# Kernel optimization log

Measured on AMD Instinct MI355X. Metric: run time of the kernel, lower is better.

## Reference

```python
import jax, jax.numpy as jnp
import numpy as np

B, T, N, U = 16, 512, 2048, 64  # batch_size, dim1, dim2 (=nodes), units


def setup_inputs() -> dict:
    key = jax.random.key(0)
    k1, k2, k3, k4 = jax.random.split(key, 4)
    x = jax.random.normal(k1, (B, T, N), dtype=jnp.float32)
    Adj = jax.random.uniform(k2, (N, N), dtype=jnp.float32)
    W = jax.random.normal(k3, (U, N), dtype=jnp.float32) * 0.05  # 'uniform' init stand-in
    b = jax.random.normal(k4, (U,), dtype=jnp.float32) * 0.05
    return {"x": x, "Adj": Adj, "W": W, "b": b}


def reference(x, Adj, W, b):
    # Original loop: out_i[b,t,j] = sum_k x[b,t,k] * Adj[j,k] * W[i,k] + b[i],
    # then mean over i. By linearity this equals a single matmul with the
    # unit-averaged weight vector and the averaged bias.
    w_bar = jnp.mean(W, axis=0)              # [N]
    w_eff = Adj * w_bar                       # [N(j), N(k)] : Adj[j,k] * w_bar[k]
    out = jnp.einsum('btk,jk->btj', x, w_eff) + jnp.mean(b)
    return out  # [B, T, N]
```

## Files before the change

### kernel.cpp

```cpp
#include <hip/hip_runtime.h>

#define N_DIM 2048
#define U_DIM 64
#define M_DIM 8192
#define K_DIM 2048

typedef __bf16 bf16x8 __attribute__((ext_vector_type(8)));
typedef float  floatx4 __attribute__((ext_vector_type(4)));
typedef unsigned short ushort8 __attribute__((ext_vector_type(8)));

#define AS1 __attribute__((address_space(1)))
#define AS3 __attribute__((address_space(3)))

__device__ __forceinline__ unsigned short f_to_bf16_rne(float f) {
    unsigned int x;
    __builtin_memcpy(&x, &f, 4);
    x += 0x7fffu + ((x >> 16) & 1u);
    return (unsigned short)(x >> 16);
}

__global__ __launch_bounds__(256) void prep_kernel(
    const float* __restrict__ W, const float* __restrict__ b,
    float* __restrict__ wbar, float* __restrict__ bmean) {
    int k = blockIdx.x * 256 + threadIdx.x;
    float s = 0.f;
#pragma unroll
    for (int i = 0; i < U_DIM; ++i) s += W[i * N_DIM + k];
    wbar[k] = s * (1.f / U_DIM);

    if (blockIdx.x == 0 && threadIdx.x < 64) {
        float v = b[threadIdx.x];
#pragma unroll
        for (int off = 32; off > 0; off >>= 1) v += __shfl_down(v, off);
        if (threadIdx.x == 0) bmean[0] = v * (1.f / U_DIM);
    }
}

__global__ __launch_bounds__(256) void weff_convx_kernel(
    const float* __restrict__ Adj, const float* __restrict__ wbar,
    unsigned short* __restrict__ weff,
    const float* __restrict__ x, unsigned short* __restrict__ xbf) {
    if (blockIdx.x < 2048) {
        long long idx = ((long long)blockIdx.x * 256 + threadIdx.x) * 8;
        int k = (int)(idx & (N_DIM - 1));
        floatx4 a0 = *(const floatx4*)(Adj + idx);
        floatx4 a1 = *(const floatx4*)(Adj + idx + 4);
        floatx4 w0 = *(const floatx4*)(wbar + k);
        floatx4 w1 = *(const floatx4*)(wbar + k + 4);
        ushort8 ov;
#pragma unroll
        for (int j = 0; j < 4; ++j) {
            ov[j]     = f_to_bf16_rne(a0[j] * w0[j]);
            ov[j + 4] = f_to_bf16_rne(a1[j] * w1[j]);
        }
        *(ushort8*)(weff + idx) = ov;
    } else {
        long long idx = ((long long)(blockIdx.x - 2048) * 256 + threadIdx.x) * 8;
        floatx4 a0 = *(const floatx4*)(x + idx);
        floatx4 a1 = *(const floatx4*)(x + idx + 4);
        ushort8 ov;
#pragma unroll
        for (int j = 0; j < 4; ++j) {
            ov[j]     = f_to_bf16_rne(a0[j]);
            ov[j + 4] = f_to_bf16_rne(a1[j]);
        }
        *(ushort8*)(xbf + idx) = ov;
    }
}

__global__ __launch_bounds__(256) void convx_kernel(
    const float* __restrict__ x, unsigned short* __restrict__ xbf) {
    long long idx = ((long long)blockIdx.x * 256 + threadIdx.x) * 8;
    floatx4 a0 = *(const floatx4*)(x + idx);
    floatx4 a1 = *(const floatx4*)(x + idx + 4);
    ushort8 ov;
#pragma unroll
    for (int j = 0; j < 4; ++j) {
        ov[j]     = f_to_bf16_rne(a0[j]);
        ov[j + 4] = f_to_bf16_rne(a1[j]);
    }
    *(ushort8*)(xbf + idx) = ov;
}

#define BM 256
#define BN 256
#define BK 64
#define NT (K_DIM / BK)

__global__ __launch_bounds__(512, 2) void gemm_bt_kernel(
    const unsigned short* __restrict__ A,
    const unsigned short* __restrict__ Bt,
    const float* __restrict__ bmeanp,
    float* __restrict__ C,
    int mtiles) {
    __shared__ __align__(16) unsigned short sA[2][BM * BK];
    __shared__ __align__(16) unsigned short sB[2][BN * BK];

    const int id   = blockIdx.x;
    const int nt   = id & 7;
    const int mt   = id >> 3;
    const int tile_m = mt * BM;
    const int tile_n = nt * BN;

    const int tid  = threadIdx.x;
    const int w    = tid >> 6;
    const int lane = tid & 63;
    const int wm   = w >> 2;
    const int wn   = w & 3;

    const float bmean = bmeanp[0];

    const int srow = lane >> 3;
    const int skc  = (lane & 7) ^ srow;
    const unsigned short* gA0 = A  + (size_t)(tile_m + w * 32 + srow) * K_DIM + skc * 8;
    const unsigned short* gB0 = Bt + (size_t)(tile_n + w * 32 + srow) * K_DIM + skc * 8;

    const int fr = lane & 15;
    const int fq = lane >> 4;
    int aoff[2], boff[2];
#pragma unroll
    for (int s = 0; s < 2; ++s) {
        int slot = ((s * 4 + fq) ^ (fr & 7)) * 8;
        aoff[s] = (wm * 128 + fr) * BK + slot;
        boff[s] = (wn * 64 + fr) * BK + slot;
    }

    floatx4 acc[8][4];
#pragma unroll
    for (int mi = 0; mi < 8; ++mi)
#pragma unroll
        for (int ni = 0; ni < 4; ++ni) acc[mi][ni] = (floatx4){0.f, 0.f, 0.f, 0.f};

    #define STAGE(p, kt)                                                          \
        do {                                                                      \
            const int koff_ = (kt) * BK;                                          \
            _Pragma("unroll")                                                     \
            for (int i_ = 0; i_ < 4; ++i_) {                                      \
                __builtin_amdgcn_global_load_lds(                                 \
                    (const AS1 void*)(gA0 + koff_ + (size_t)i_ * 8 * K_DIM),      \
                    (AS3 void*)(&sA[(p)][(w * 4 + i_) * 8 * BK]), 16, 0, 0);      \
                __builtin_amdgcn_global_load_lds(                                 \
                    (const AS1 void*)(gB0 + koff_ + (size_t)i_ * 8 * K_DIM),      \
                    (AS3 void*)(&sB[(p)][(w * 4 + i_) * 8 * BK]), 16, 0, 0);      \
            }                                                                     \
        } while (0)

    STAGE(0, 0);
    STAGE(1, 1);

    for (int t = 0; t < NT; ++t) {
        const int p = t & 1;

        if (t == NT - 1) asm volatile("s_waitcnt vmcnt(0)" ::: "memory");
        else             asm volatile("s_waitcnt vmcnt(8)" ::: "memory");
        __builtin_amdgcn_s_barrier();

#pragma unroll
        for (int s = 0; s < 2; ++s) {
            bf16x8 af[8], bfr[4];
#pragma unroll
            for (int mi = 0; mi < 8; ++mi)
                af[mi] = *(const bf16x8*)&sA[p][aoff[s] + mi * 16 * BK];
#pragma unroll
            for (int ni = 0; ni < 4; ++ni)
                bfr[ni] = *(const bf16x8*)&sB[p][boff[s] + ni * 16 * BK];
            asm volatile("s_waitcnt lgkmcnt(0)" ::: "memory");
            __builtin_amdgcn_sched_barrier(0);
            __builtin_amdgcn_s_setprio(1);
#pragma unroll
            for (int mi = 0; mi < 8; ++mi)
#pragma unroll
                for (int ni = 0; ni < 4; ++ni)
                    acc[mi][ni] = __builtin_amdgcn_mfma_f32_16x16x32_bf16(
                        af[mi], bfr[ni], acc[mi][ni], 0, 0, 0);
            __builtin_amdgcn_s_setprio(0);
        }

        __builtin_amdgcn_s_barrier();

        if (t + 2 < NT) STAGE(p, t + 2);
    }
    #undef STAGE

    const int crow = tile_m + wm * 128 + fq * 4;
    const int ccol = tile_n + wn * 64 + fr;
#pragma unroll
    for (int mi = 0; mi < 8; ++mi)
#pragma unroll
        for (int ni = 0; ni < 4; ++ni)
#pragma unroll
            for (int r = 0; r < 4; ++r) {
                int gm = crow + mi * 16 + r;
                int gn = ccol + ni * 16;
                C[(size_t)gm * N_DIM + gn] = acc[mi][ni][r] + bmean;
            }
    (void)mtiles;
}

extern "C" void kernel_launch(void* const* d_in, const int* in_sizes, int n_in,
                              void* d_out, int out_size, void* d_ws, size_t ws_size,
                              hipStream_t stream) {
    (void)in_sizes; (void)n_in; (void)out_size;
    const float* x   = (const float*)d_in[0];
    const float* Adj = (const float*)d_in[1];
    const float* W   = (const float*)d_in[2];
    const float* b   = (const float*)d_in[3];
    float* out = (float*)d_out;

    char* ws = (char*)d_ws;
    float* wbar  = (float*)ws;
    float* bmean = (float*)(ws + 8192);
    unsigned short* weff = (unsigned short*)(ws + 16384);
    const size_t weff_bytes = (size_t)N_DIM * N_DIM * 2;
    const size_t xbf_off = 16384 + weff_bytes;
    unsigned short* xbf = (unsigned short*)(ws + xbf_off);

    size_t avail = (ws_size > xbf_off) ? (ws_size - xbf_off) : 0;
    long long max_rows = (long long)(avail / ((size_t)K_DIM * 2)) / BM * BM;
    if (max_rows < BM) max_rows = BM;
    if (max_rows > M_DIM) max_rows = M_DIM;

    prep_kernel<<<N_DIM / 256, 256, 0, stream>>>(W, b, wbar, bmean);

    if (max_rows == M_DIM) {
        weff_convx_kernel<<<2048 + M_DIM, 256, 0, stream>>>(Adj, wbar, weff, x, xbf);
        gemm_bt_kernel<<<(M_DIM / BM) * (N_DIM / BN), 512, 0, stream>>>(
            xbf, weff, bmean, out, M_DIM / BM);
    } else {
        weff_convx_kernel<<<2048, 256, 0, stream>>>(Adj, wbar, weff, x, xbf);
        for (long long m0 = 0; m0 < M_DIM; m0 += max_rows) {
            long long rows = (M_DIM - m0 < max_rows) ? (M_DIM - m0) : max_rows;
            convx_kernel<<<(int)rows, 256, 0, stream>>>(x + m0 * K_DIM, xbf);
            gemm_bt_kernel<<<(int)(rows / BM) * (N_DIM / BN), 512, 0, stream>>>(
                xbf, weff, bmean, out + m0 * (size_t)N_DIM, (int)(rows / BM));
        }
    }
}
```

Baseline: 224.5 us.

## Interleave LDS fragment reads with MFMA groups and issue next stage early

Splits each K-tile's work into four MFMA groups and interleaves the LDS fragment loads for the next group with the current group's MFMAs, so LDS latency overlaps with matrix math. The last MFMA group runs after the barrier and after the global-to-LDS prefetch is issued, so the next stage's loads start earlier. This raises register pressure (more fragments live at once) and relies on sched_barrier placement, which may cause spills or lower occupancy at 2 blocks per CU.

```diff
diff --git a/kernel.cpp b/kernel.cpp
--- a/kernel.cpp
+++ b/kernel.cpp
@@ -155,30 +155,71 @@
         else             asm volatile("s_waitcnt vmcnt(8)" ::: "memory");
         __builtin_amdgcn_s_barrier();
 
-#pragma unroll
-        for (int s = 0; s < 2; ++s) {
-            bf16x8 af[8], bfr[4];
-#pragma unroll
-            for (int mi = 0; mi < 8; ++mi)
-                af[mi] = *(const bf16x8*)&sA[p][aoff[s] + mi * 16 * BK];
-#pragma unroll
-            for (int ni = 0; ni < 4; ++ni)
-                bfr[ni] = *(const bf16x8*)&sB[p][boff[s] + ni * 16 * BK];
-            asm volatile("s_waitcnt lgkmcnt(0)" ::: "memory");
-            __builtin_amdgcn_sched_barrier(0);
-            __builtin_amdgcn_s_setprio(1);
-#pragma unroll
-            for (int mi = 0; mi < 8; ++mi)
-#pragma unroll
-                for (int ni = 0; ni < 4; ++ni)
-                    acc[mi][ni] = __builtin_amdgcn_mfma_f32_16x16x32_bf16(
-                        af[mi], bfr[ni], acc[mi][ni], 0, 0, 0);
-            __builtin_amdgcn_s_setprio(0);
-        }
-
+        bf16x8 bf0[4], bf1[4], afa[4], afb[4], afc[4], afd[4];
+
+#pragma unroll
+        for (int ni = 0; ni < 4; ++ni)
+            bf0[ni] = *(const bf16x8*)&sB[p][boff[0] + ni * 16 * BK];
+#pragma unroll
+        for (int i = 0; i < 4; ++i)
+            afa[i] = *(const bf16x8*)&sA[p][aoff[0] + i * 16 * BK];
+        __builtin_amdgcn_sched_barrier(0);
+
+#pragma unroll
+        for (int i = 0; i < 4; ++i)
+            afb[i] = *(const bf16x8*)&sA[p][aoff[0] + (4 + i) * 16 * BK];
+#pragma unroll
+        for (int ni = 0; ni < 4; ++ni)
+            bf1[ni] = *(const bf16x8*)&sB[p][boff[1] + ni * 16 * BK];
+        __builtin_amdgcn_sched_barrier(0);
+        __builtin_amdgcn_s_setprio(1);
+#pragma unroll
+        for (int mi = 0; mi < 4; ++mi)
+#pragma unroll
+            for (int ni = 0; ni < 4; ++ni)
+                acc[mi][ni] = __builtin_amdgcn_mfma_f32_16x16x32_bf16(
+                    afa[mi], bf0[ni], acc[mi][ni], 0, 0, 0);
+        __builtin_amdgcn_s_setprio(0);
+
+#pragma unroll
+        for (int i = 0; i < 4; ++i)
+            afc[i] = *(const bf16x8*)&sA[p][aoff[1] + i * 16 * BK];
+        __builtin_amdgcn_sched_barrier(0);
+        __builtin_amdgcn_s_setprio(1);
+#pragma unroll
+        for (int mi = 4; mi < 8; ++mi)
+#pragma unroll
+            for (int ni = 0; ni < 4; ++ni)
+                acc[mi][ni] = __builtin_amdgcn_mfma_f32_16x16x32_bf16(
+                    afb[mi - 4], bf0[ni], acc[mi][ni], 0, 0, 0);
+        __builtin_amdgcn_s_setprio(0);
+
+#pragma unroll
+        for (int i = 0; i < 4; ++i)
+            afd[i] = *(const bf16x8*)&sA[p][aoff[1] + (4 + i) * 16 * BK];
+        __builtin_amdgcn_sched_barrier(0);
+        __builtin_amdgcn_s_setprio(1);
+#pragma unroll
+        for (int mi = 0; mi < 4; ++mi)
+#pragma unroll
+            for (int ni = 0; ni < 4; ++ni)
+                acc[mi][ni] = __builtin_amdgcn_mfma_f32_16x16x32_bf16(
+                    afc[mi], bf1[ni], acc[mi][ni], 0, 0, 0);
+        __builtin_amdgcn_s_setprio(0);
+
+        asm volatile("s_waitcnt lgkmcnt(0)" ::: "memory");
+        __builtin_amdgcn_sched_barrier(0);
         __builtin_amdgcn_s_barrier();
-
         if (t + 2 < NT) STAGE(p, t + 2);
+        __builtin_amdgcn_sched_barrier(0);
+        __builtin_amdgcn_s_setprio(1);
+#pragma unroll
+        for (int mi = 4; mi < 8; ++mi)
+#pragma unroll
+            for (int ni = 0; ni < 4; ++ni)
+                acc[mi][ni] = __builtin_amdgcn_mfma_f32_16x16x32_bf16(
+                    afd[mi - 4], bf1[ni], acc[mi][ni], 0, 0, 0);
+        __builtin_amdgcn_s_setprio(0);
     }
     #undef STAGE
 
```

Result: faster. 217.4 us (-3.2%).

## Split GEMM main loop into four quadrant phases with interleaved half-tile prefetch

Applied to the files above, without the earlier changes.

Restructures the bf16 GEMM inner loop into four MFMA phases over 4x2 sub-quadrants of each warp's accumulator tile. Global-to-LDS loads for the next k-tile are issued in half-tile chunks spread across the phases, and LDS fragment reads are interleaved between them, in the style of ping-pong scheduling. The goal is to hide load latency and smooth out memory traffic against MFMA execution. In exchange it adds many more barriers per iteration and more complex vmcnt/lgkmcnt accounting, which carries a correctness risk.

```diff
diff --git a/kernel.cpp b/kernel.cpp
--- a/kernel.cpp
+++ b/kernel.cpp
@@ -112,8 +112,8 @@
 
     const int srow = lane >> 3;
     const int skc  = (lane & 7) ^ srow;
-    const unsigned short* gA0 = A  + (size_t)(tile_m + w * 32 + srow) * K_DIM + skc * 8;
-    const unsigned short* gB0 = Bt + (size_t)(tile_n + w * 32 + srow) * K_DIM + skc * 8;
+    const unsigned short* gA = A  + (size_t)(tile_m + w * 16 + srow) * K_DIM + skc * 8;
+    const unsigned short* gB = Bt + (size_t)(tile_n + w * 16 + srow) * K_DIM + skc * 8;
 
     const int fr = lane & 15;
     const int fq = lane >> 4;
@@ -131,56 +131,134 @@
 #pragma unroll
         for (int ni = 0; ni < 4; ++ni) acc[mi][ni] = (floatx4){0.f, 0.f, 0.f, 0.f};
 
-    #define STAGE(p, kt)                                                          \
-        do {                                                                      \
-            const int koff_ = (kt) * BK;                                          \
-            _Pragma("unroll")                                                     \
-            for (int i_ = 0; i_ < 4; ++i_) {                                      \
-                __builtin_amdgcn_global_load_lds(                                 \
-                    (const AS1 void*)(gA0 + koff_ + (size_t)i_ * 8 * K_DIM),      \
-                    (AS3 void*)(&sA[(p)][(w * 4 + i_) * 8 * BK]), 16, 0, 0);      \
-                __builtin_amdgcn_global_load_lds(                                 \
-                    (const AS1 void*)(gB0 + koff_ + (size_t)i_ * 8 * K_DIM),      \
-                    (AS3 void*)(&sB[(p)][(w * 4 + i_) * 8 * BK]), 16, 0, 0);      \
-            }                                                                     \
+    #define STAGE_A_HALF(p, kt, h)                                                 \
+        do {                                                                       \
+            const int ko_ = (kt) * BK;                                             \
+            _Pragma("unroll")                                                      \
+            for (int u_ = 0; u_ < 2; ++u_) {                                       \
+                __builtin_amdgcn_global_load_lds(                                  \
+                    (const AS1 void*)(gA + ko_ +                                   \
+                        (size_t)((h) * 128 + u_ * 8) * K_DIM),                     \
+                    (AS3 void*)(&sA[(p)][((h) * 128 + w * 16 + u_ * 8) * BK]),     \
+                    16, 0, 0);                                                     \
+            }                                                                      \
         } while (0)
-
-    STAGE(0, 0);
-    STAGE(1, 1);
+    #define STAGE_B_HALF(p, kt, h)                                                 \
+        do {                                                                       \
+            const int ko_ = (kt) * BK;                                             \
+            _Pragma("unroll")                                                      \
+            for (int u_ = 0; u_ < 2; ++u_) {                                       \
+                __builtin_amdgcn_global_load_lds(                                  \
+                    (const AS1 void*)(gB + ko_ +                                   \
+                        (size_t)((h) * 128 + u_ * 8) * K_DIM),                     \
+                    (AS3 void*)(&sB[(p)][((h) * 128 + w * 16 + u_ * 8) * BK]),     \
+                    16, 0, 0);                                                     \
+            }                                                                      \
+        } while (0)
+
+    STAGE_A_HALF(0, 0, 0);
+    STAGE_A_HALF(0, 0, 1);
+    STAGE_B_HALF(0, 0, 0);
+    STAGE_B_HALF(0, 0, 1);
+    STAGE_A_HALF(1, 1, 0);
+    asm volatile("s_waitcnt vmcnt(2)" ::: "memory");
+    __builtin_amdgcn_s_barrier();
 
     for (int t = 0; t < NT; ++t) {
         const int p = t & 1;
-
-        if (t == NT - 1) asm volatile("s_waitcnt vmcnt(0)" ::: "memory");
-        else             asm volatile("s_waitcnt vmcnt(8)" ::: "memory");
-        __builtin_amdgcn_s_barrier();
+        const int q = p ^ 1;
+        bf16x8 a0[4][2], a1[4][2], b0[2][2], b1[2][2];
 
 #pragma unroll
         for (int s = 0; s < 2; ++s) {
-            bf16x8 af[8], bfr[4];
-#pragma unroll
-            for (int mi = 0; mi < 8; ++mi)
-                af[mi] = *(const bf16x8*)&sA[p][aoff[s] + mi * 16 * BK];
-#pragma unroll
-            for (int ni = 0; ni < 4; ++ni)
-                bfr[ni] = *(const bf16x8*)&sB[p][boff[s] + ni * 16 * BK];
-            asm volatile("s_waitcnt lgkmcnt(0)" ::: "memory");
-            __builtin_amdgcn_sched_barrier(0);
-            __builtin_amdgcn_s_setprio(1);
-#pragma unroll
-            for (int mi = 0; mi < 8; ++mi)
-#pragma unroll
-                for (int ni = 0; ni < 4; ++ni)
+#pragma unroll
+            for (int mi = 0; mi < 4; ++mi)
+                a0[mi][s] = *(const bf16x8*)&sA[p][aoff[s] + mi * 16 * BK];
+#pragma unroll
+            for (int ni = 0; ni < 2; ++ni)
+                b0[ni][s] = *(const bf16x8*)&sB[p][boff[s] + ni * 16 * BK];
+        }
+        if (t + 1 < NT) STAGE_A_HALF(q, t + 1, 1);
+        asm volatile("s_waitcnt lgkmcnt(8)" ::: "memory");
+        __builtin_amdgcn_s_barrier();
+        asm volatile("s_waitcnt lgkmcnt(0)" ::: "memory");
+        __builtin_amdgcn_sched_barrier(0);
+        __builtin_amdgcn_s_setprio(1);
+#pragma unroll
+        for (int s = 0; s < 2; ++s)
+#pragma unroll
+            for (int mi = 0; mi < 4; ++mi)
+#pragma unroll
+                for (int ni = 0; ni < 2; ++ni)
                     acc[mi][ni] = __builtin_amdgcn_mfma_f32_16x16x32_bf16(
-                        af[mi], bfr[ni], acc[mi][ni], 0, 0, 0);
-            __builtin_amdgcn_s_setprio(0);
-        }
-
-        __builtin_amdgcn_s_barrier();
-
-        if (t + 2 < NT) STAGE(p, t + 2);
-    }
-    #undef STAGE
+                        a0[mi][s], b0[ni][s], acc[mi][ni], 0, 0, 0);
+        __builtin_amdgcn_s_setprio(0);
+        __builtin_amdgcn_s_barrier();
+
+#pragma unroll
+        for (int s = 0; s < 2; ++s)
+#pragma unroll
+            for (int ni = 0; ni < 2; ++ni)
+                b1[ni][s] = *(const bf16x8*)&sB[p][boff[s] + (2 + ni) * 16 * BK];
+        if (t + 1 < NT) STAGE_B_HALF(q, t + 1, 0);
+        __builtin_amdgcn_s_barrier();
+        asm volatile("s_waitcnt lgkmcnt(0)" ::: "memory");
+        __builtin_amdgcn_sched_barrier(0);
+        __builtin_amdgcn_s_setprio(1);
+#pragma unroll
+        for (int s = 0; s < 2; ++s)
+#pragma unroll
+            for (int mi = 0; mi < 4; ++mi)
+#pragma unroll
+                for (int ni = 0; ni < 2; ++ni)
+                    acc[mi][2 + ni] = __builtin_amdgcn_mfma_f32_16x16x32_bf16(
+                        a0[mi][s], b1[ni][s], acc[mi][2 + ni], 0, 0, 0);
+        __builtin_amdgcn_s_setprio(0);
+        __builtin_amdgcn_s_barrier();
+
+#pragma unroll
+        for (int s = 0; s < 2; ++s)
+#pragma unroll
+            for (int mi = 0; mi < 4; ++mi)
+                a1[mi][s] = *(const bf16x8*)&sA[p][aoff[s] + (4 + mi) * 16 * BK];
+        if (t + 1 < NT) STAGE_B_HALF(q, t + 1, 1);
+        __builtin_amdgcn_s_barrier();
+        asm volatile("s_waitcnt lgkmcnt(0)" ::: "memory");
+        __builtin_amdgcn_sched_barrier(0);
+        __builtin_amdgcn_s_setprio(1);
+#pragma unroll
+        for (int s = 0; s < 2; ++s)
+#pragma unroll
+            for (int mi = 0; mi < 4; ++mi)
+#pragma unroll
+                for (int ni = 0; ni < 2; ++ni)
+                    acc[4 + mi][ni] = __builtin_amdgcn_mfma_f32_16x16x32_bf16(
+                        a1[mi][s], b0[ni][s], acc[4 + mi][ni], 0, 0, 0);
+        __builtin_amdgcn_s_setprio(0);
+        __builtin_amdgcn_s_barrier();
+
+        if (t + 2 < NT) {
+            STAGE_A_HALF(p, t + 2, 0);
+            asm volatile("s_waitcnt vmcnt(2)" ::: "memory");
+        } else {
+            asm volatile("s_waitcnt vmcnt(0)" ::: "memory");
+        }
+        __builtin_amdgcn_s_barrier();
+        __builtin_amdgcn_sched_barrier(0);
+        __builtin_amdgcn_s_setprio(1);
+#pragma unroll
+        for (int s = 0; s < 2; ++s)
+#pragma unroll
+            for (int mi = 0; mi < 4; ++mi)
+#pragma unroll
+                for (int ni = 0; ni < 2; ++ni)
+                    acc[4 + mi][2 + ni] = __builtin_amdgcn_mfma_f32_16x16x32_bf16(
+                        a1[mi][s], b1[ni][s], acc[4 + mi][2 + ni], 0, 0, 0);
+        __builtin_amdgcn_s_setprio(0);
+        __builtin_amdgcn_s_barrier();
+    }
+    #undef STAGE_A_HALF
+    #undef STAGE_B_HALF
 
     const int crow = tile_m + wm * 128 + fq * 4;
     const int ccol = tile_n + wn * 64 + fr;
```

New measurement: 227.9 us. Within noise of the previous version (+1.5%).

## Load B fragments directly into registers and shrink GEMM tile to 128x256

Applied to the files above, without the earlier changes.

The GEMM now uses 4 waves over a 128x256 tile. Only the A operand is staged in LDS. The weight operand (B) is loaded straight from global memory into registers, double-buffered across K steps, which removes the B LDS traffic and its footprint. Each wave now owns a 64-column slice across the full 128 rows. The cost is more register pressure, uncoalesced-ish direct global loads for B, and twice as many blocks reloading B.

```diff
diff --git a/kernel.cpp b/kernel.cpp
--- a/kernel.cpp
+++ b/kernel.cpp
@@ -82,19 +82,18 @@
     *(ushort8*)(xbf + idx) = ov;
 }
 
-#define BM 256
+#define BM 128
 #define BN 256
 #define BK 64
 #define NT (K_DIM / BK)
 
-__global__ __launch_bounds__(512, 2) void gemm_bt_kernel(
+__global__ __launch_bounds__(256, 2) void gemm_bt_kernel(
     const unsigned short* __restrict__ A,
     const unsigned short* __restrict__ Bt,
     const float* __restrict__ bmeanp,
     float* __restrict__ C,
     int mtiles) {
     __shared__ __align__(16) unsigned short sA[2][BM * BK];
-    __shared__ __align__(16) unsigned short sB[2][BN * BK];
 
     const int id   = blockIdx.x;
     const int nt   = id & 7;
@@ -105,25 +104,24 @@
     const int tid  = threadIdx.x;
     const int w    = tid >> 6;
     const int lane = tid & 63;
-    const int wm   = w >> 2;
-    const int wn   = w & 3;
 
     const float bmean = bmeanp[0];
 
     const int srow = lane >> 3;
     const int skc  = (lane & 7) ^ srow;
-    const unsigned short* gA0 = A  + (size_t)(tile_m + w * 32 + srow) * K_DIM + skc * 8;
-    const unsigned short* gB0 = Bt + (size_t)(tile_n + w * 32 + srow) * K_DIM + skc * 8;
+    const unsigned short* gA0 = A + (size_t)(tile_m + w * 32 + srow) * K_DIM + skc * 8;
 
     const int fr = lane & 15;
     const int fq = lane >> 4;
-    int aoff[2], boff[2];
-#pragma unroll
-    for (int s = 0; s < 2; ++s) {
-        int slot = ((s * 4 + fq) ^ (fr & 7)) * 8;
-        aoff[s] = (wm * 128 + fr) * BK + slot;
-        boff[s] = (wn * 64 + fr) * BK + slot;
-    }
+    int aoff[2];
+#pragma unroll
+    for (int s = 0; s < 2; ++s)
+        aoff[s] = fr * BK + (((s * 4 + fq) ^ (fr & 7)) * 8);
+
+    const unsigned short* pB[4];
+#pragma unroll
+    for (int ni = 0; ni < 4; ++ni)
+        pB[ni] = Bt + (size_t)(tile_n + w * 64 + ni * 16 + fr) * K_DIM + fq * 8;
 
     floatx4 acc[8][4];
 #pragma unroll
@@ -131,59 +129,75 @@
 #pragma unroll
         for (int ni = 0; ni < 4; ++ni) acc[mi][ni] = (floatx4){0.f, 0.f, 0.f, 0.f};
 
-    #define STAGE(p, kt)                                                          \
+    #define STAGE_A(p, kt)                                                        \
         do {                                                                      \
-            const int koff_ = (kt) * BK;                                          \
+            const int ko_ = (kt) * BK;                                            \
             _Pragma("unroll")                                                     \
             for (int i_ = 0; i_ < 4; ++i_) {                                      \
                 __builtin_amdgcn_global_load_lds(                                 \
-                    (const AS1 void*)(gA0 + koff_ + (size_t)i_ * 8 * K_DIM),      \
+                    (const AS1 void*)(gA0 + ko_ + (size_t)i_ * 8 * K_DIM),        \
                     (AS3 void*)(&sA[(p)][(w * 4 + i_) * 8 * BK]), 16, 0, 0);      \
-                __builtin_amdgcn_global_load_lds(                                 \
-                    (const AS1 void*)(gB0 + koff_ + (size_t)i_ * 8 * K_DIM),      \
-                    (AS3 void*)(&sB[(p)][(w * 4 + i_) * 8 * BK]), 16, 0, 0);      \
             }                                                                     \
         } while (0)
 
-    STAGE(0, 0);
-    STAGE(1, 1);
-
-    for (int t = 0; t < NT; ++t) {
-        const int p = t & 1;
-
-        if (t == NT - 1) asm volatile("s_waitcnt vmcnt(0)" ::: "memory");
-        else             asm volatile("s_waitcnt vmcnt(8)" ::: "memory");
-        __builtin_amdgcn_s_barrier();
-
-#pragma unroll
-        for (int s = 0; s < 2; ++s) {
-            bf16x8 af[8], bfr[4];
-#pragma unroll
-            for (int mi = 0; mi < 8; ++mi)
-                af[mi] = *(const bf16x8*)&sA[p][aoff[s] + mi * 16 * BK];
-#pragma unroll
-            for (int ni = 0; ni < 4; ++ni)
-                bfr[ni] = *(const bf16x8*)&sB[p][boff[s] + ni * 16 * BK];
-            asm volatile("s_waitcnt lgkmcnt(0)" ::: "memory");
-            __builtin_amdgcn_sched_barrier(0);
-            __builtin_amdgcn_s_setprio(1);
-#pragma unroll
-            for (int mi = 0; mi < 8; ++mi)
-#pragma unroll
-                for (int ni = 0; ni < 4; ++ni)
-                    acc[mi][ni] = __builtin_amdgcn_mfma_f32_16x16x32_bf16(
-                        af[mi], bfr[ni], acc[mi][ni], 0, 0, 0);
-            __builtin_amdgcn_s_setprio(0);
-        }
-
-        __builtin_amdgcn_s_barrier();
-
-        if (t + 2 < NT) STAGE(p, t + 2);
-    }
-    #undef STAGE
-
-    const int crow = tile_m + wm * 128 + fq * 4;
-    const int ccol = tile_n + wn * 64 + fr;
+    #define BODY(T, RB_CUR, RB_NXT)                                               \
+        do {                                                                      \
+            const int t_ = (T);                                                   \
+            const int p_ = t_ & 1;                                                \
+            if (t_ + 1 < NT) {                                                    \
+                _Pragma("unroll")                                                 \
+                for (int ni = 0; ni < 4; ++ni) {                                  \
+                    _Pragma("unroll")                                             \
+                    for (int s = 0; s < 2; ++s)                                   \
+                        RB_NXT[ni][s] =                                           \
+                            *(const bf16x8*)(pB[ni] + BK + s * 32);               \
+                }                                                                 \
+            }                                                                     \
+            if (t_ == NT - 1) asm volatile("s_waitcnt vmcnt(0)" ::: "memory");    \
+            else              asm volatile("s_waitcnt vmcnt(12)" ::: "memory");   \
+            __builtin_amdgcn_s_barrier();                     \
+            _Pragma("unroll")                                                     \
+            for (int s = 0; s < 2; ++s) {                                         \
+                bf16x8 af[8];                                                     \
+                _Pragma("unroll")                                                 \
+                for (int mi = 0; mi < 8; ++mi)                                    \
+                    af[mi] = *(const bf16x8*)&sA[p_][aoff[s] + mi * 16 * BK];     \
+                asm volatile("s_waitcnt lgkmcnt(0)" ::: "memory");                \
+                __builtin_amdgcn_sched_barrier(0);                                \
+                __builtin_amdgcn_s_setprio(1);                                    \
+                _Pragma("unroll")                                                 \
+                for (int mi = 0; mi < 8; ++mi) {                                  \
+                    _Pragma("unroll")                                             \
+                    for (int ni = 0; ni < 4; ++ni)                                \
+                        acc[mi][ni] = __builtin_amdgcn_mfma_f32_16x16x32_bf16(    \
+                            af[mi], RB_CUR[ni][s], acc[mi][ni], 0, 0, 0);         \
+                }                                                                 \
+                __builtin_amdgcn_s_setprio(0);                                    \
+            }                                                                     \
+            __builtin_amdgcn_s_barrier();                      \
+            if (t_ + 2 < NT) STAGE_A(p_, t_ + 2);                                 \
+            _Pragma("unroll")                                                     \
+            for (int ni = 0; ni < 4; ++ni) pB[ni] += BK;                          \
+        } while (0)
+
+    bf16x8 rb0[4][2], rb1[4][2];
+#pragma unroll
+    for (int ni = 0; ni < 4; ++ni)
+#pragma unroll
+        for (int s = 0; s < 2; ++s)
+            rb0[ni][s] = *(const bf16x8*)(pB[ni] + s * 32);
+    STAGE_A(0, 0);
+    STAGE_A(1, 1);
+
+    for (int tt = 0; tt < NT; tt += 2) {
+        BODY(tt,     rb0, rb1);
+        BODY(tt + 1, rb1, rb0);
+    }
+    #undef BODY
+    #undef STAGE_A
+
+    const int crow = tile_m + fq * 4;
+    const int ccol = tile_n + w * 64 + fr;
 #pragma unroll
     for (int mi = 0; mi < 8; ++mi)
 #pragma unroll
@@ -224,14 +238,14 @@
 
     if (max_rows == M_DIM) {
         weff_convx_kernel<<<2048 + M_DIM, 256, 0, stream>>>(Adj, wbar, weff, x, xbf);
-        gemm_bt_kernel<<<(M_DIM / BM) * (N_DIM / BN), 512, 0, stream>>>(
+        gemm_bt_kernel<<<(M_DIM / BM) * (N_DIM / BN), 256, 0, stream>>>(
             xbf, weff, bmean, out, M_DIM / BM);
     } else {
         weff_convx_kernel<<<2048, 256, 0, stream>>>(Adj, wbar, weff, x, xbf);
         for (long long m0 = 0; m0 < M_DIM; m0 += max_rows) {
             long long rows = (M_DIM - m0 < max_rows) ? (M_DIM - m0) : max_rows;
             convx_kernel<<<(int)rows, 256, 0, stream>>>(x + m0 * K_DIM, xbf);
-            gemm_bt_kernel<<<(int)(rows / BM) * (N_DIM / BN), 512, 0, stream>>>(
+            gemm_bt_kernel<<<(int)(rows / BM) * (N_DIM / BN), 256, 0, stream>>>(
                 xbf, weff, bmean, out + m0 * (size_t)N_DIM, (int)(rows / BM));
         }
     }
```

After: 311.0 us. 1.39x slower.
